# Kernel tuning notes

Hardware: AMD Instinct MI355X
Metric: run time of the kernel (lower is better)

## Reference

```python
import jax, jax.numpy as jnp
import numpy as np
import math

B, T, S = 32, 512, 256          # batch, tgt_len (prediction_length), src_len (encoder tokens)
PD, ED = 1, 768                 # pred_dim, encoder_dim
D, H, L, FF = 256, 8, 4, 1024   # d_model, nhead, num_layers, dim_feedforward
HD = D // H
NEG = -1e9
EPS = 1e-5


def _pos_encoding(seq_len, d_model):
    pos = jnp.arange(seq_len, dtype=jnp.float32)[:, None]
    div = jnp.exp(jnp.arange(0, d_model, 2, dtype=jnp.float32) * (-math.log(10000.0) / d_model))
    pe = jnp.zeros((seq_len, d_model), jnp.float32)
    pe = pe.at[:, 0::2].set(jnp.sin(pos * div))
    pe = pe.at[:, 1::2].set(jnp.cos(pos * div))
    return pe


def _ln(x, g, b):
    m = jnp.mean(x, -1, keepdims=True)
    v = jnp.mean((x - m) ** 2, -1, keepdims=True)
    return (x - m) * jax.lax.rsqrt(v + EPS) * g + b


def _mha(xq, xkv, Wq, bq, Wk, bk, Wv, bv, Wo, bo, mask):
    b, t, d = xq.shape
    s = xkv.shape[1]
    Q = (xq @ Wq + bq).reshape(b, t, H, HD).transpose(0, 2, 1, 3)   # bhtd
    K = (xkv @ Wk + bk).reshape(b, s, H, HD).transpose(0, 2, 1, 3)  # bhsd
    V = (xkv @ Wv + bv).reshape(b, s, H, HD).transpose(0, 2, 1, 3)
    scores = jnp.einsum('bhtd,bhsd->bhts', Q, K) * (HD ** -0.5)
    if mask is not None:
        scores = scores + mask
    w = jax.nn.softmax(scores, axis=-1)
    o = jnp.einsum('bhts,bhsd->bhtd', w, V).transpose(0, 2, 1, 3).reshape(b, t, d)
    return o @ Wo + bo


def _forward(tgt, memory, W_emb, b_emb, W_enc, b_enc,
             Wq_s, bq_s, Wk_s, bk_s, Wv_s, bv_s, Wo_s, bo_s,
             Wq_c, bq_c, Wk_c, bk_c, Wv_c, bv_c, Wo_c, bo_c,
             g1, be1, g2, be2, g3, be3, Wf1, bf1, Wf2, bf2,
             Wp1, bp1, Wp2, bp2):
    t = tgt.shape[1]
    x = tgt @ W_emb + b_emb + _pos_encoding(t, D)          # (B,T,D)
    mem = memory @ W_enc + b_enc                           # (B,S,D)
    causal = jnp.triu(jnp.full((t, t), NEG, jnp.float32), k=1)
    for i in range(L):
        sa = _mha(x, x, Wq_s[i], bq_s[i], Wk_s[i], bk_s[i], Wv_s[i], bv_s[i], Wo_s[i], bo_s[i], causal)
        x = _ln(x + sa, g1[i], be1[i])
        ca = _mha(x, mem, Wq_c[i], bq_c[i], Wk_c[i], bk_c[i], Wv_c[i], bv_c[i], Wo_c[i], bo_c[i], None)
        x = _ln(x + ca, g2[i], be2[i])
        ff = jax.nn.gelu(x @ Wf1[i] + bf1[i], approximate=False) @ Wf2[i] + bf2[i]
        x = _ln(x + ff, g3[i], be3[i])
    h = jax.nn.gelu(x @ Wp1 + bp1, approximate=False)
    return h @ Wp2 + bp2                                   # (B,T,PD)


def setup_inputs() -> dict:
    key = jax.random.key(0)
    keys = iter(jax.random.split(key, 40))
    def rn(shape, scale=0.05):
        return jax.random.normal(next(keys), shape, jnp.float32) * scale
    z = jnp.zeros
    inp = {
        'tgt': jax.random.normal(next(keys), (B, T, PD), jnp.float32),
        'memory': jax.random.normal(next(keys), (B, S, ED), jnp.float32),
        'W_emb': rn((PD, D)), 'b_emb': z((D,)),
        'W_enc': rn((ED, D)), 'b_enc': z((D,)),
        'Wq_s': rn((L, D, D)), 'bq_s': z((L, D)),
        'Wk_s': rn((L, D, D)), 'bk_s': z((L, D)),
        'Wv_s': rn((L, D, D)), 'bv_s': z((L, D)),
        'Wo_s': rn((L, D, D)), 'bo_s': z((L, D)),
        'Wq_c': rn((L, D, D)), 'bq_c': z((L, D)),
        'Wk_c': rn((L, D, D)), 'bk_c': z((L, D)),
        'Wv_c': rn((L, D, D)), 'bv_c': z((L, D)),
        'Wo_c': rn((L, D, D)), 'bo_c': z((L, D)),
        'g1': jnp.ones((L, D)), 'be1': z((L, D)),
        'g2': jnp.ones((L, D)), 'be2': z((L, D)),
        'g3': jnp.ones((L, D)), 'be3': z((L, D)),
        'Wf1': rn((L, D, FF)), 'bf1': z((L, FF)),
        'Wf2': rn((L, FF, D)), 'bf2': z((L, D)),
        'Wp1': rn((D, D // 2)), 'bp1': z((D // 2,)),
        'Wp2': rn((D // 2, PD), 0.01), 'bp2': jnp.full((PD,), 0.1, jnp.float32),
    }
    return inp


def reference(tgt, memory, W_emb, b_emb, W_enc, b_enc,
              Wq_s, bq_s, Wk_s, bk_s, Wv_s, bv_s, Wo_s, bo_s,
              Wq_c, bq_c, Wk_c, bk_c, Wv_c, bv_c, Wo_c, bo_c,
              g1, be1, g2, be2, g3, be3, Wf1, bf1, Wf2, bf2,
              Wp1, bp1, Wp2, bp2):
    return _forward(tgt, memory, W_emb, b_emb, W_enc, b_enc,
                    Wq_s, bq_s, Wk_s, bk_s, Wv_s, bv_s, Wo_s, bo_s,
                    Wq_c, bq_c, Wk_c, bk_c, Wv_c, bv_c, Wo_c, bo_c,
                    g1, be1, g2, be2, g3, be3, Wf1, bf1, Wf2, bf2,
                    Wp1, bp1, Wp2, bp2)
```

## Files before the change

kernel.cpp:

```cpp
#include <hip/hip_runtime.h>
#include <math.h>

#define B_  32
#define T_  512
#define S_  256
#define D_  256
#define H_  8
#define HD_ 32
#define FF_ 1024
#define ED_ 768
#define L_  4
#define BT_ (B_*T_)
#define BS_ (B_*S_)

typedef __bf16 bf16x8_t __attribute__((ext_vector_type(8)));
typedef __bf16 bf16x4_t __attribute__((ext_vector_type(4)));
typedef float  f32x4_t  __attribute__((ext_vector_type(4)));

__device__ __forceinline__ float gelu_f(float v) {
  return 0.5f * v * (1.f + erff(v * 0.7071067811865476f));
}

__device__ __forceinline__ void gl16(const __bf16* gsrc, __bf16* ldst) {
  __builtin_amdgcn_global_load_lds(
      (const __attribute__((address_space(1))) unsigned int*)gsrc,
      (__attribute__((address_space(3))) unsigned int*)ldst, 16, 0, 0);
}

__global__ __launch_bounds__(256)
void embed_kernel(const float* __restrict__ tgt, const float* __restrict__ Wemb,
                  const float* __restrict__ bemb, float* __restrict__ x,
                  __bf16* __restrict__ xbf) {
  int i = blockIdx.x * 256 + threadIdx.x;
  int d  = i & (D_ - 1);
  int bt = i >> 8;
  int t  = bt & (T_ - 1);
  int p  = d >> 1;
  float div = expf((float)(2 * p) * (-9.210340371976184f / (float)D_));
  float arg = (float)t * div;
  float pe = (d & 1) ? cosf(arg) : sinf(arg);
  float v = tgt[bt] * Wemb[d] + bemb[d] + pe;
  x[i] = v;
  xbf[i] = (__bf16)v;
}

__global__ __launch_bounds__(256)
void cvt_bf16_kernel(const float* __restrict__ in, __bf16* __restrict__ out) {
  int i = (blockIdx.x * 256 + threadIdx.x) * 4;
  float4 v = *(const float4*)(in + i);
  bf16x4_t o;
  o[0] = (__bf16)v.x; o[1] = (__bf16)v.y; o[2] = (__bf16)v.z; o[3] = (__bf16)v.w;
  *(bf16x4_t*)(out + i) = o;
}

struct TD { const float* src; size_t dst; int K, N, nb; size_t lstride; };
struct TDs { TD d[12]; };

__global__ __launch_bounds__(256)
void transpose_cvt_kernel(TDs a, __bf16* __restrict__ wt) {
  __shared__ float tile[32][33];
  TD t = a.d[blockIdx.y];
  const int kt = t.K >> 5, nt = t.N >> 5;
  const int per = kt * nt, tot = per * t.nb;
  const int id = blockIdx.x;
  if (id >= tot) return;
  const int b = id / per;
  const int r2 = id - b * per;
  const int kti = r2 / nt;
  const int nti = r2 - kti * nt;
  const int c = threadIdx.x & 31, r0 = threadIdx.x >> 5;
  const float* src = t.src + (size_t)b * t.K * t.N;
  __bf16* dst = wt + t.dst + (size_t)b * t.lstride;
#pragma unroll
  for (int j = 0; j < 4; ++j) {
    int rr = r0 + j * 8;
    tile[rr][c] = src[(size_t)(kti * 32 + rr) * t.N + nti * 32 + c];
  }
  __syncthreads();
#pragma unroll
  for (int j = 0; j < 4; ++j) {
    int rr = r0 + j * 8;
    dst[(size_t)(nti * 32 + rr) * t.K + kti * 32 + c] = (__bf16)tile[c][rr];
  }
}

__global__ __launch_bounds__(256)
void bias_concat_kernel(const float* __restrict__ bq_s, const float* __restrict__ bk_s,
                        const float* __restrict__ bv_s, const float* __restrict__ bk_c,
                        const float* __restrict__ bv_c, float* __restrict__ dst) {
  int idx = blockIdx.x * 256 + threadIdx.x;
  if (idx >= 5120) return;
  if (idx < 3072) {
    int l = idx / 768, c = idx - l * 768;
    float v = (c < 256) ? bq_s[l * 256 + c]
            : (c < 512) ? bk_s[l * 256 + c - 256]
                        : bv_s[l * 256 + c - 512];
    dst[idx] = v;
  } else {
    int j = idx - 3072;
    int l = j / 512, c = j - l * 512;
    float v = (c < 256) ? bk_c[l * 256 + c] : bv_c[l * 256 + c - 256];
    dst[idx] = v;
  }
}

template<int ACT, int OBF>
__global__ __launch_bounds__(256, 3)
void gemm_bf(const __bf16* __restrict__ A, const __bf16* __restrict__ Bt,
             const float* __restrict__ bias, void* __restrict__ Cv,
             int N, int K, int nN, int ppx) {
  __shared__ __bf16 As[128 * 64];
  __shared__ __bf16 Bs[64 * 64];
  const int tid = threadIdx.x, lane = tid & 63, wv = tid >> 6;
  const int wm = (wv & 1) * 64, wn = (wv >> 1) * 32;
  const int ln15 = lane & 15, kgrp = lane >> 4;
  const int xcd = blockIdx.x & 7, j = blockIdx.x >> 3;
  const int bm = (xcd * ppx + j / nN) * 128;
  const int bn = (j % nN) * 64;

  const int r8 = lane >> 3;
  const int scol = (lane & 7) ^ r8;
  const __bf16* a_g = A  + (size_t)(bm + wv * 32 + r8) * K + scol * 8;
  const __bf16* b_g = Bt + (size_t)(bn + wv * 16 + r8) * K + scol * 8;
  __bf16* a_l = As + wv * 2048;
  __bf16* b_l = Bs + wv * 1024;

  const int xk0 = kgrp ^ (ln15 & 7);
  const int xk1 = (4 + kgrp) ^ (ln15 & 7);

  f32x4_t acc[4][2];
#pragma unroll
  for (int mi = 0; mi < 4; ++mi)
#pragma unroll
    for (int ni = 0; ni < 2; ++ni) acc[mi][ni] = (f32x4_t){0.f, 0.f, 0.f, 0.f};

  for (int k0 = 0; k0 < K; k0 += 64) {
    gl16(a_g + k0,                a_l);
    gl16(a_g + k0 + (size_t)8*K,  a_l + 512);
    gl16(a_g + k0 + (size_t)16*K, a_l + 1024);
    gl16(a_g + k0 + (size_t)24*K, a_l + 1536);
    gl16(b_g + k0,                b_l);
    gl16(b_g + k0 + (size_t)8*K,  b_l + 512);
    __syncthreads();

#pragma unroll
    for (int kk = 0; kk < 2; ++kk) {
      const int xk = kk ? xk1 : xk0;
      bf16x8_t b0 = *(const bf16x8_t*)(Bs + ((wn + ln15) * 8 + xk) * 8);
      bf16x8_t b1 = *(const bf16x8_t*)(Bs + ((wn + 16 + ln15) * 8 + xk) * 8);
#pragma unroll
      for (int mi = 0; mi < 4; ++mi) {
        bf16x8_t af = *(const bf16x8_t*)(As + ((wm + mi * 16 + ln15) * 8 + xk) * 8);
        acc[mi][0] = __builtin_amdgcn_mfma_f32_16x16x32_bf16(af, b0, acc[mi][0], 0, 0, 0);
        acc[mi][1] = __builtin_amdgcn_mfma_f32_16x16x32_bf16(af, b1, acc[mi][1], 0, 0, 0);
      }
    }
    __syncthreads();
  }

#pragma unroll
  for (int mi = 0; mi < 4; ++mi) {
#pragma unroll
    for (int ni = 0; ni < 2; ++ni) {
      const int ocol = bn + wn + ni * 16 + ln15;
      const float bv = bias[ocol];
      const int orow0 = bm + wm + mi * 16 + kgrp * 4;
#pragma unroll
      for (int r = 0; r < 4; ++r) {
        float o = acc[mi][ni][r] + bv;
        if (ACT == 1) o = gelu_f(o);
        if (OBF) ((__bf16*)Cv)[(size_t)(orow0 + r) * N + ocol] = (__bf16)o;
        else     ((float*)Cv)[(size_t)(orow0 + r) * N + ocol] = o;
      }
    }
  }
}

template<bool CAUSAL>
__global__ __launch_bounds__(256)
void attn_mfma(const __bf16* __restrict__ Q, const __bf16* __restrict__ K,
               const __bf16* __restrict__ V, __bf16* __restrict__ O,
               int KVROWS, int qs, int ks) {
  const int b = blockIdx.x >> 3, h = blockIdx.x & 7;
  const int qt = blockIdx.y;
  const int tid = threadIdx.x, lane = tid & 63, wv = tid >> 6;
  const int ln15 = lane & 15, kgrp = lane >> 4, kgrp8 = kgrp * 8;

  __shared__ __bf16 K_lds[32][40];
  __shared__ __bf16 Vt_lds[32][40];
  __shared__ __bf16 P_lds[4][16][40];

  const int q_glob = qt * 64 + wv * 16 + ln15;
  const bf16x8_t qfrag = *(const bf16x8_t*)(Q + (size_t)(b * T_ + q_glob) * qs + h * HD_ + kgrp8);

  const int s_r = tid >> 3, s_c = (tid & 7) * 4;
  const __bf16* Kb = K + (size_t)(b * KVROWS + s_r) * ks + h * HD_ + s_c;
  const __bf16* Vb = V + (size_t)(b * KVROWS + s_r) * ks + h * HD_ + s_c;

  f32x4_t o0 = (f32x4_t){0.f,0.f,0.f,0.f}, o1 = (f32x4_t){0.f,0.f,0.f,0.f};
  float m = -3.0e38f, l = 0.f;
  const float SCALE = 0.17677669529663689f;
  const int slim = CAUSAL ? (qt + 1) * 64 : KVROWS;

  for (int s0 = 0; s0 < slim; s0 += 32) {
    *(uint2*)&K_lds[s_r][s_c] = *(const uint2*)(Kb + (size_t)s0 * ks);
    bf16x4_t vv = *(const bf16x4_t*)(Vb + (size_t)s0 * ks);
    Vt_lds[s_c + 0][s_r] = vv[0];
    Vt_lds[s_c + 1][s_r] = vv[1];
    Vt_lds[s_c + 2][s_r] = vv[2];
    Vt_lds[s_c + 3][s_r] = vv[3];
    __syncthreads();

    bf16x8_t kf0 = *(const bf16x8_t*)&K_lds[ln15][kgrp8];
    bf16x8_t kf1 = *(const bf16x8_t*)&K_lds[16 + ln15][kgrp8];
    f32x4_t sa0 = (f32x4_t){0.f,0.f,0.f,0.f}, sa1 = (f32x4_t){0.f,0.f,0.f,0.f};
    sa0 = __builtin_amdgcn_mfma_f32_16x16x32_bf16(kf0, qfrag, sa0, 0, 0, 0);
    sa1 = __builtin_amdgcn_mfma_f32_16x16x32_bf16(kf1, qfrag, sa1, 0, 0, 0);

    float v[8];
#pragma unroll
    for (int r = 0; r < 4; ++r) { v[r] = sa0[r] * SCALE; v[4 + r] = sa1[r] * SCALE; }
    if (CAUSAL) {
      const int sb = s0 + kgrp * 4;
#pragma unroll
      for (int r = 0; r < 4; ++r) {
        if (sb + r      > q_glob) v[r]     += -1e9f;
        if (sb + 16 + r > q_glob) v[4 + r] += -1e9f;
      }
    }
    float tmax = v[0];
#pragma unroll
    for (int r = 1; r < 8; ++r) tmax = fmaxf(tmax, v[r]);
    tmax = fmaxf(tmax, __shfl_xor(tmax, 16));
    tmax = fmaxf(tmax, __shfl_xor(tmax, 32));
    float mnew = fmaxf(m, tmax);
    float corr = __expf(m - mnew);

    float lsum = 0.f;
    bf16x4_t p0, p1;
#pragma unroll
    for (int r = 0; r < 4; ++r) {
      float e0 = __expf(v[r] - mnew);
      float e1 = __expf(v[4 + r] - mnew);
      lsum += e0 + e1;
      p0[r] = (__bf16)e0;
      p1[r] = (__bf16)e1;
    }
    *(bf16x4_t*)&P_lds[wv][ln15][kgrp * 4]      = p0;
    *(bf16x4_t*)&P_lds[wv][ln15][16 + kgrp * 4] = p1;
    lsum += __shfl_xor(lsum, 16);
    lsum += __shfl_xor(lsum, 32);
    l = l * corr + lsum;
    m = mnew;

    const float c0 = __shfl(corr, kgrp * 4 + 0);
    const float c1 = __shfl(corr, kgrp * 4 + 1);
    const float c2 = __shfl(corr, kgrp * 4 + 2);
    const float c3 = __shfl(corr, kgrp * 4 + 3);
    o0[0] *= c0; o0[1] *= c1; o0[2] *= c2; o0[3] *= c3;
    o1[0] *= c0; o1[1] *= c1; o1[2] *= c2; o1[3] *= c3;

    bf16x8_t pf  = *(const bf16x8_t*)&P_lds[wv][ln15][kgrp8];
    bf16x8_t vf0 = *(const bf16x8_t*)&Vt_lds[ln15][kgrp8];
    bf16x8_t vf1 = *(const bf16x8_t*)&Vt_lds[16 + ln15][kgrp8];
    o0 = __builtin_amdgcn_mfma_f32_16x16x32_bf16(pf, vf0, o0, 0, 0, 0);
    o1 = __builtin_amdgcn_mfma_f32_16x16x32_bf16(pf, vf1, o1, 0, 0, 0);
    __syncthreads();
  }

  const float inv = 1.f / l;
  const float i0 = __shfl(inv, kgrp * 4 + 0);
  const float i1 = __shfl(inv, kgrp * 4 + 1);
  const float i2 = __shfl(inv, kgrp * 4 + 2);
  const float i3 = __shfl(inv, kgrp * 4 + 3);
  __bf16* Op = O + (size_t)(b * T_ + qt * 64 + wv * 16 + kgrp * 4) * D_ + h * HD_;
  Op[0 * D_ + ln15] = (__bf16)(o0[0] * i0);  Op[0 * D_ + 16 + ln15] = (__bf16)(o1[0] * i0);
  Op[1 * D_ + ln15] = (__bf16)(o0[1] * i1);  Op[1 * D_ + 16 + ln15] = (__bf16)(o1[1] * i1);
  Op[2 * D_ + ln15] = (__bf16)(o0[2] * i2);  Op[2 * D_ + 16 + ln15] = (__bf16)(o1[2] * i2);
  Op[3 * D_ + ln15] = (__bf16)(o0[3] * i3);  Op[3 * D_ + 16 + ln15] = (__bf16)(o1[3] * i3);
}

__global__ __launch_bounds__(256)
void add_ln_kernel(float* __restrict__ x, __bf16* __restrict__ xbf,
                   const float* __restrict__ y,
                   const float* __restrict__ g, const float* __restrict__ bta) {
  const int row = blockIdx.x * 4 + (threadIdx.x >> 6);
  const int lane = threadIdx.x & 63;
  const size_t base = (size_t)row * D_ + lane * 4;
  float4 xv = *(const float4*)&x[base];
  float4 yv = *(const float4*)&y[base];
  float v0 = xv.x + yv.x, v1 = xv.y + yv.y, v2 = xv.z + yv.z, v3 = xv.w + yv.w;
  float sum = v0 + v1 + v2 + v3;
  float sq  = v0 * v0 + v1 * v1 + v2 * v2 + v3 * v3;
#pragma unroll
  for (int off = 32; off; off >>= 1) {
    sum += __shfl_xor(sum, off);
    sq  += __shfl_xor(sq, off);
  }
  float mean = sum * (1.f / D_);
  float var  = sq * (1.f / D_) - mean * mean;
  float rstd = rsqrtf(fmaxf(var, 0.f) + 1e-5f);
  const int c = lane * 4;
  float4 gv = *(const float4*)&g[c];
  float4 bv = *(const float4*)&bta[c];
  float4 ov;
  ov.x = (v0 - mean) * rstd * gv.x + bv.x;
  ov.y = (v1 - mean) * rstd * gv.y + bv.y;
  ov.z = (v2 - mean) * rstd * gv.z + bv.z;
  ov.w = (v3 - mean) * rstd * gv.w + bv.w;
  *(float4*)&x[base] = ov;
  bf16x4_t ob;
  ob[0] = (__bf16)ov.x; ob[1] = (__bf16)ov.y; ob[2] = (__bf16)ov.z; ob[3] = (__bf16)ov.w;
  *(bf16x4_t*)&xbf[base] = ob;
}

__global__ __launch_bounds__(256)
void head2_kernel(const float* __restrict__ hb, const float* __restrict__ w,
                  const float* __restrict__ bias, float* __restrict__ out) {
  const int row = blockIdx.x * 4 + (threadIdx.x >> 6);
  const int lane = threadIdx.x & 63;
  float a = hb[(size_t)row * 128 + lane] * w[lane]
          + hb[(size_t)row * 128 + 64 + lane] * w[64 + lane];
#pragma unroll
  for (int off = 32; off; off >>= 1) a += __shfl_xor(a, off);
  if (lane == 0) out[row] = a + bias[0];
}

extern "C" void kernel_launch(void* const* d_in, const int* in_sizes, int n_in,
                              void* d_out, int out_size, void* d_ws, size_t ws_size,
                              hipStream_t stream) {
  const float* tgt    = (const float*)d_in[0];
  const float* memory = (const float*)d_in[1];
  const float* W_emb  = (const float*)d_in[2];
  const float* b_emb  = (const float*)d_in[3];
  const float* W_enc  = (const float*)d_in[4];
  const float* b_enc  = (const float*)d_in[5];
  const float* Wq_s = (const float*)d_in[6];  const float* bq_s = (const float*)d_in[7];
  const float* Wk_s = (const float*)d_in[8];  const float* bk_s = (const float*)d_in[9];
  const float* Wv_s = (const float*)d_in[10]; const float* bv_s = (const float*)d_in[11];
  const float* Wo_s = (const float*)d_in[12]; const float* bo_s = (const float*)d_in[13];
  const float* Wq_c = (const float*)d_in[14]; const float* bq_c = (const float*)d_in[15];
  const float* Wk_c = (const float*)d_in[16]; const float* bk_c = (const float*)d_in[17];
  const float* Wv_c = (const float*)d_in[18]; const float* bv_c = (const float*)d_in[19];
  const float* Wo_c = (const float*)d_in[20]; const float* bo_c = (const float*)d_in[21];
  const float* g1  = (const float*)d_in[22]; const float* be1 = (const float*)d_in[23];
  const float* g2  = (const float*)d_in[24]; const float* be2 = (const float*)d_in[25];
  const float* g3  = (const float*)d_in[26]; const float* be3 = (const float*)d_in[27];
  const float* Wf1 = (const float*)d_in[28]; const float* bf1 = (const float*)d_in[29];
  const float* Wf2 = (const float*)d_in[30]; const float* bf2 = (const float*)d_in[31];
  const float* Wp1 = (const float*)d_in[32]; const float* bp1 = (const float*)d_in[33];
  const float* Wp2 = (const float*)d_in[34]; const float* bp2 = (const float*)d_in[35];

  float*  x    = (float*)d_ws;
  float*  y    = x + (size_t)BT_ * D_;
  __bf16* xbf  = (__bf16*)(y + (size_t)BT_ * D_);
  __bf16* membf= xbf + (size_t)BT_ * D_;
  __bf16* qkv  = membf + (size_t)BS_ * D_;
  __bf16* ext  = qkv + (size_t)BT_ * 768;
  __bf16* ao   = ext + (size_t)4194304;
  __bf16* wt   = ao + (size_t)BT_ * D_;
  float*  bcat = (float*)(wt + 4423680);
  __bf16* memb = qkv;
  __bf16* qc   = qkv;
  __bf16* kvc  = qkv + (size_t)BT_ * D_;
  __bf16* ff   = qkv;

  const size_t o_enc  = 0;
  const size_t o_qkv  = 196608;
  const size_t o_qcw  = 983040;
  const size_t o_kvw  = 1245184;
  const size_t o_os   = 1769472;
  const size_t o_oc   = 2031616;
  const size_t o_f1   = 2293760;
  const size_t o_f2   = 3342336;
  const size_t o_p1   = 4390912;

  TDs td;
  td.d[0]  = {W_enc, o_enc,           ED_, D_,  1, 0};
  td.d[1]  = {Wq_s,  o_qkv + 0,       D_,  D_,  L_, 196608};
  td.d[2]  = {Wk_s,  o_qkv + 65536,   D_,  D_,  L_, 196608};
  td.d[3]  = {Wv_s,  o_qkv + 131072,  D_,  D_,  L_, 196608};
  td.d[4]  = {Wq_c,  o_qcw,           D_,  D_,  L_, 65536};
  td.d[5]  = {Wk_c,  o_kvw + 0,       D_,  D_,  L_, 131072};
  td.d[6]  = {Wv_c,  o_kvw + 65536,   D_,  D_,  L_, 131072};
  td.d[7]  = {Wo_s,  o_os,            D_,  D_,  L_, 65536};
  td.d[8]  = {Wo_c,  o_oc,            D_,  D_,  L_, 65536};
  td.d[9]  = {Wf1,   o_f1,            D_,  FF_, L_, 262144};
  td.d[10] = {Wf2,   o_f2,            FF_, D_,  L_, 262144};
  td.d[11] = {Wp1,   o_p1,            D_,  128, 1, 0};

  dim3 blk(256);
  cvt_bf16_kernel<<<BS_ * ED_ / 1024, blk, 0, stream>>>(memory, memb);
  transpose_cvt_kernel<<<dim3(1024, 12), blk, 0, stream>>>(td, wt);
  bias_concat_kernel<<<20, blk, 0, stream>>>(bq_s, bk_s, bv_s, bk_c, bv_c, bcat);
  embed_kernel<<<BT_ * D_ / 256, blk, 0, stream>>>(tgt, W_emb, b_emb, x, xbf);

  const float* bqkv = bcat;
  const float* bkv  = bcat + 3072;
  const dim3 gA(B_ * H_, T_ / 64);

  gemm_bf<0,1><<<64 * 4, blk, 0, stream>>>(memb, wt + o_enc, b_enc, membf, D_, ED_, 4, 8);

  for (int i = 0; i < L_; ++i) {
    gemm_bf<0,1><<<128 * 12, blk, 0, stream>>>(xbf, wt + o_qkv + (size_t)i * 196608, bqkv + i * 768, qkv, 768, D_, 12, 16);
    attn_mfma<true><<<gA, blk, 0, stream>>>(qkv, qkv + 256, qkv + 512, ao, T_, 768, 768);
    gemm_bf<0,0><<<128 * 4, blk, 0, stream>>>(ao, wt + o_os + (size_t)i * 65536, bo_s + i * D_, y, D_, D_, 4, 16);
    add_ln_kernel<<<BT_ / 4, blk, 0, stream>>>(x, xbf, y, g1 + i * D_, be1 + i * D_);
    gemm_bf<0,1><<<128 * 4, blk, 0, stream>>>(xbf, wt + o_qcw + (size_t)i * 65536, bq_c + i * D_, qc, D_, D_, 4, 16);
    gemm_bf<0,1><<<64 * 8, blk, 0, stream>>>(membf, wt + o_kvw + (size_t)i * 131072, bkv + i * 512, kvc, 512, D_, 8, 8);
    attn_mfma<false><<<gA, blk, 0, stream>>>(qc, kvc, kvc + 256, ao, S_, 256, 512);
    gemm_bf<0,0><<<128 * 4, blk, 0, stream>>>(ao, wt + o_oc + (size_t)i * 65536, bo_c + i * D_, y, D_, D_, 4, 16);
    add_ln_kernel<<<BT_ / 4, blk, 0, stream>>>(x, xbf, y, g2 + i * D_, be2 + i * D_);
    gemm_bf<1,1><<<128 * 16, blk, 0, stream>>>(xbf, wt + o_f1 + (size_t)i * 262144, bf1 + i * FF_, ff, FF_, D_, 16, 16);
    gemm_bf<0,0><<<128 * 4, blk, 0, stream>>>(ff, wt + o_f2 + (size_t)i * 262144, bf2 + i * D_, y, D_, FF_, 4, 16);
    add_ln_kernel<<<BT_ / 4, blk, 0, stream>>>(x, xbf, y, g3 + i * D_, be3 + i * D_);
  }
  gemm_bf<1,0><<<128 * 2, blk, 0, stream>>>(xbf, wt + o_p1, bp1, y, 128, D_, 2, 16);
  head2_kernel<<<BT_ / 4, blk, 0, stream>>>(y, Wp2, bp2, (float*)d_out);
}
```

Before: 752.3 us.

## Add 128x128 GEMM tile, widen attention KV tile, store residual branch in bf16

Adds a gemm_bf2 kernel with 128x128 output tiles and a 4x4 MFMA grid per wave, and uses it for the QKV and FF1 projections. The larger tiles raise operand reuse and halve the number of blocks for those GEMMs. Attention now processes 64 keys per iteration instead of 32, with 8-wide vector K/V loads, which halves the loop trips and barrier count. The output, cross-attention and FF2 projections now write their result in bf16 and add_ln reads bf16, cutting that traffic in half. The cost is lower precision in the residual branch and more register pressure in the new GEMM.

```diff
diff --git a/kernel.cpp b/kernel.cpp
--- a/kernel.cpp
+++ b/kernel.cpp
@@ -176,6 +176,83 @@
   }
 }
 
+template<int ACT, int OBF>
+__global__ __launch_bounds__(256, 3)
+void gemm_bf2(const __bf16* __restrict__ A, const __bf16* __restrict__ Bt,
+              const float* __restrict__ bias, void* __restrict__ Cv,
+              int N, int K, int nN, int ppx) {
+  __shared__ __bf16 As[128 * 64];
+  __shared__ __bf16 Bs[128 * 64];
+  const int tid = threadIdx.x, lane = tid & 63, wv = tid >> 6;
+  const int wm = (wv & 1) * 64, wn = (wv >> 1) * 64;
+  const int ln15 = lane & 15, kgrp = lane >> 4;
+  const int xcd = blockIdx.x & 7, j = blockIdx.x >> 3;
+  const int bm = (xcd * ppx + j / nN) * 128;
+  const int bn = (j % nN) * 128;
+
+  const int r8 = lane >> 3;
+  const int scol = (lane & 7) ^ r8;
+  const __bf16* a_g = A  + (size_t)(bm + wv * 32 + r8) * K + scol * 8;
+  const __bf16* b_g = Bt + (size_t)(bn + wv * 32 + r8) * K + scol * 8;
+  __bf16* a_l = As + wv * 2048;
+  __bf16* b_l = Bs + wv * 2048;
+
+  const int xk0 = kgrp ^ (ln15 & 7);
+  const int xk1 = (4 + kgrp) ^ (ln15 & 7);
+
+  f32x4_t acc[4][4];
+#pragma unroll
+  for (int mi = 0; mi < 4; ++mi)
+#pragma unroll
+    for (int ni = 0; ni < 4; ++ni) acc[mi][ni] = (f32x4_t){0.f, 0.f, 0.f, 0.f};
+
+  for (int k0 = 0; k0 < K; k0 += 64) {
+    gl16(a_g + k0,                a_l);
+    gl16(a_g + k0 + (size_t)8*K,  a_l + 512);
+    gl16(a_g + k0 + (size_t)16*K, a_l + 1024);
+    gl16(a_g + k0 + (size_t)24*K, a_l + 1536);
+    gl16(b_g + k0,                b_l);
+    gl16(b_g + k0 + (size_t)8*K,  b_l + 512);
+    gl16(b_g + k0 + (size_t)16*K, b_l + 1024);
+    gl16(b_g + k0 + (size_t)24*K, b_l + 1536);
+    __syncthreads();
+
+#pragma unroll
+    for (int kk = 0; kk < 2; ++kk) {
+      const int xk = kk ? xk1 : xk0;
+      bf16x8_t bfr[4];
+#pragma unroll
+      for (int ni = 0; ni < 4; ++ni)
+        bfr[ni] = *(const bf16x8_t*)(Bs + ((wn + ni * 16 + ln15) * 8 + xk) * 8);
+#pragma unroll
+      for (int mi = 0; mi < 4; ++mi) {
+        bf16x8_t af = *(const bf16x8_t*)(As + ((wm + mi * 16 + ln15) * 8 + xk) * 8);
+#pragma unroll
+        for (int ni = 0; ni < 4; ++ni)
+          acc[mi][ni] = __builtin_amdgcn_mfma_f32_16x16x32_bf16(af, bfr[ni], acc[mi][ni], 0, 0, 0);
+      }
+    }
+    __syncthreads();
+  }
+
+#pragma unroll
+  for (int mi = 0; mi < 4; ++mi) {
+#pragma unroll
+    for (int ni = 0; ni < 4; ++ni) {
+      const int ocol = bn + wn + ni * 16 + ln15;
+      const float bv = bias[ocol];
+      const int orow0 = bm + wm + mi * 16 + kgrp * 4;
+#pragma unroll
+      for (int r = 0; r < 4; ++r) {
+        float o = acc[mi][ni][r] + bv;
+        if (ACT == 1) o = gelu_f(o);
+        if (OBF) ((__bf16*)Cv)[(size_t)(orow0 + r) * N + ocol] = (__bf16)o;
+        else     ((float*)Cv)[(size_t)(orow0 + r) * N + ocol] = o;
+      }
+    }
+  }
+}
+
 template<bool CAUSAL>
 __global__ __launch_bounds__(256)
 void attn_mfma(const __bf16* __restrict__ Q, const __bf16* __restrict__ K,
@@ -186,68 +263,64 @@
   const int tid = threadIdx.x, lane = tid & 63, wv = tid >> 6;
   const int ln15 = lane & 15, kgrp = lane >> 4, kgrp8 = kgrp * 8;
 
-  __shared__ __bf16 K_lds[32][40];
-  __shared__ __bf16 Vt_lds[32][40];
-  __shared__ __bf16 P_lds[4][16][40];
+  __shared__ __bf16 K_lds[64][36];
+  __shared__ __bf16 Vt_lds[32][72];
+  __shared__ __bf16 P_lds[4][16][72];
 
   const int q_glob = qt * 64 + wv * 16 + ln15;
   const bf16x8_t qfrag = *(const bf16x8_t*)(Q + (size_t)(b * T_ + q_glob) * qs + h * HD_ + kgrp8);
 
-  const int s_r = tid >> 3, s_c = (tid & 7) * 4;
-  const __bf16* Kb = K + (size_t)(b * KVROWS + s_r) * ks + h * HD_ + s_c;
-  const __bf16* Vb = V + (size_t)(b * KVROWS + s_r) * ks + h * HD_ + s_c;
+  const int s_r = tid >> 2, s_c8 = (tid & 3) * 8;
+  const __bf16* Kb = K + (size_t)(b * KVROWS + s_r) * ks + h * HD_ + s_c8;
+  const __bf16* Vb = V + (size_t)(b * KVROWS + s_r) * ks + h * HD_ + s_c8;
 
   f32x4_t o0 = (f32x4_t){0.f,0.f,0.f,0.f}, o1 = (f32x4_t){0.f,0.f,0.f,0.f};
   float m = -3.0e38f, l = 0.f;
   const float SCALE = 0.17677669529663689f;
   const int slim = CAUSAL ? (qt + 1) * 64 : KVROWS;
 
-  for (int s0 = 0; s0 < slim; s0 += 32) {
-    *(uint2*)&K_lds[s_r][s_c] = *(const uint2*)(Kb + (size_t)s0 * ks);
-    bf16x4_t vv = *(const bf16x4_t*)(Vb + (size_t)s0 * ks);
-    Vt_lds[s_c + 0][s_r] = vv[0];
-    Vt_lds[s_c + 1][s_r] = vv[1];
-    Vt_lds[s_c + 2][s_r] = vv[2];
-    Vt_lds[s_c + 3][s_r] = vv[3];
+  for (int s0 = 0; s0 < slim; s0 += 64) {
+    *(bf16x8_t*)&K_lds[s_r][s_c8] = *(const bf16x8_t*)(Kb + (size_t)s0 * ks);
+    bf16x8_t vv = *(const bf16x8_t*)(Vb + (size_t)s0 * ks);
+#pragma unroll
+    for (int jj = 0; jj < 8; ++jj) Vt_lds[s_c8 + jj][s_r] = vv[jj];
     __syncthreads();
 
-    bf16x8_t kf0 = *(const bf16x8_t*)&K_lds[ln15][kgrp8];
-    bf16x8_t kf1 = *(const bf16x8_t*)&K_lds[16 + ln15][kgrp8];
-    f32x4_t sa0 = (f32x4_t){0.f,0.f,0.f,0.f}, sa1 = (f32x4_t){0.f,0.f,0.f,0.f};
-    sa0 = __builtin_amdgcn_mfma_f32_16x16x32_bf16(kf0, qfrag, sa0, 0, 0, 0);
-    sa1 = __builtin_amdgcn_mfma_f32_16x16x32_bf16(kf1, qfrag, sa1, 0, 0, 0);
-
-    float v[8];
-#pragma unroll
-    for (int r = 0; r < 4; ++r) { v[r] = sa0[r] * SCALE; v[4 + r] = sa1[r] * SCALE; }
-    if (CAUSAL) {
-      const int sb = s0 + kgrp * 4;
+    f32x4_t sa[4];
+#pragma unroll
+    for (int c = 0; c < 4; ++c) {
+      bf16x8_t kf = *(const bf16x8_t*)&K_lds[c * 16 + ln15][kgrp8];
+      sa[c] = __builtin_amdgcn_mfma_f32_16x16x32_bf16(kf, qfrag, (f32x4_t){0.f,0.f,0.f,0.f}, 0, 0, 0);
+    }
+    float v[16];
+#pragma unroll
+    for (int c = 0; c < 4; ++c)
 #pragma unroll
       for (int r = 0; r < 4; ++r) {
-        if (sb + r      > q_glob) v[r]     += -1e9f;
-        if (sb + 16 + r > q_glob) v[4 + r] += -1e9f;
+        float s = sa[c][r] * SCALE;
+        if (CAUSAL && (s0 + c * 16 + kgrp * 4 + r) > q_glob) s += -1e9f;
+        v[c * 4 + r] = s;
       }
-    }
     float tmax = v[0];
 #pragma unroll
-    for (int r = 1; r < 8; ++r) tmax = fmaxf(tmax, v[r]);
+    for (int r = 1; r < 16; ++r) tmax = fmaxf(tmax, v[r]);
     tmax = fmaxf(tmax, __shfl_xor(tmax, 16));
     tmax = fmaxf(tmax, __shfl_xor(tmax, 32));
     float mnew = fmaxf(m, tmax);
     float corr = __expf(m - mnew);
 
     float lsum = 0.f;
-    bf16x4_t p0, p1;
-#pragma unroll
-    for (int r = 0; r < 4; ++r) {
-      float e0 = __expf(v[r] - mnew);
-      float e1 = __expf(v[4 + r] - mnew);
-      lsum += e0 + e1;
-      p0[r] = (__bf16)e0;
-      p1[r] = (__bf16)e1;
+#pragma unroll
+    for (int c = 0; c < 4; ++c) {
+      bf16x4_t pc;
+#pragma unroll
+      for (int r = 0; r < 4; ++r) {
+        float e = __expf(v[c * 4 + r] - mnew);
+        lsum += e;
+        pc[r] = (__bf16)e;
+      }
+      *(bf16x4_t*)&P_lds[wv][ln15][c * 16 + kgrp * 4] = pc;
     }
-    *(bf16x4_t*)&P_lds[wv][ln15][kgrp * 4]      = p0;
-    *(bf16x4_t*)&P_lds[wv][ln15][16 + kgrp * 4] = p1;
     lsum += __shfl_xor(lsum, 16);
     lsum += __shfl_xor(lsum, 32);
     l = l * corr + lsum;
@@ -260,11 +333,16 @@
     o0[0] *= c0; o0[1] *= c1; o0[2] *= c2; o0[3] *= c3;
     o1[0] *= c0; o1[1] *= c1; o1[2] *= c2; o1[3] *= c3;
 
-    bf16x8_t pf  = *(const bf16x8_t*)&P_lds[wv][ln15][kgrp8];
-    bf16x8_t vf0 = *(const bf16x8_t*)&Vt_lds[ln15][kgrp8];
-    bf16x8_t vf1 = *(const bf16x8_t*)&Vt_lds[16 + ln15][kgrp8];
-    o0 = __builtin_amdgcn_mfma_f32_16x16x32_bf16(pf, vf0, o0, 0, 0, 0);
-    o1 = __builtin_amdgcn_mfma_f32_16x16x32_bf16(pf, vf1, o1, 0, 0, 0);
+    bf16x8_t pLo = *(const bf16x8_t*)&P_lds[wv][ln15][kgrp8];
+    bf16x8_t pHi = *(const bf16x8_t*)&P_lds[wv][ln15][32 + kgrp8];
+    bf16x8_t v0l = *(const bf16x8_t*)&Vt_lds[ln15][kgrp8];
+    bf16x8_t v0h = *(const bf16x8_t*)&Vt_lds[ln15][32 + kgrp8];
+    bf16x8_t v1l = *(const bf16x8_t*)&Vt_lds[16 + ln15][kgrp8];
+    bf16x8_t v1h = *(const bf16x8_t*)&Vt_lds[16 + ln15][32 + kgrp8];
+    o0 = __builtin_amdgcn_mfma_f32_16x16x32_bf16(pLo, v0l, o0, 0, 0, 0);
+    o0 = __builtin_amdgcn_mfma_f32_16x16x32_bf16(pHi, v0h, o0, 0, 0, 0);
+    o1 = __builtin_amdgcn_mfma_f32_16x16x32_bf16(pLo, v1l, o1, 0, 0, 0);
+    o1 = __builtin_amdgcn_mfma_f32_16x16x32_bf16(pHi, v1h, o1, 0, 0, 0);
     __syncthreads();
   }
 
@@ -282,14 +360,15 @@
 
 __global__ __launch_bounds__(256)
 void add_ln_kernel(float* __restrict__ x, __bf16* __restrict__ xbf,
-                   const float* __restrict__ y,
+                   const __bf16* __restrict__ y,
                    const float* __restrict__ g, const float* __restrict__ bta) {
   const int row = blockIdx.x * 4 + (threadIdx.x >> 6);
   const int lane = threadIdx.x & 63;
   const size_t base = (size_t)row * D_ + lane * 4;
   float4 xv = *(const float4*)&x[base];
-  float4 yv = *(const float4*)&y[base];
-  float v0 = xv.x + yv.x, v1 = xv.y + yv.y, v2 = xv.z + yv.z, v3 = xv.w + yv.w;
+  bf16x4_t yv = *(const bf16x4_t*)&y[base];
+  float v0 = xv.x + (float)yv[0], v1 = xv.y + (float)yv[1];
+  float v2 = xv.z + (float)yv[2], v3 = xv.w + (float)yv[3];
   float sum = v0 + v1 + v2 + v3;
   float sq  = v0 * v0 + v1 * v1 + v2 * v2 + v3 * v3;
 #pragma unroll
@@ -352,8 +431,9 @@
   const float* Wp2 = (const float*)d_in[34]; const float* bp2 = (const float*)d_in[35];
 
   float*  x    = (float*)d_ws;
-  float*  y    = x + (size_t)BT_ * D_;
-  __bf16* xbf  = (__bf16*)(y + (size_t)BT_ * D_);
+  float*  yf   = x + (size_t)BT_ * D_;
+  __bf16* ybf  = (__bf16*)yf;
+  __bf16* xbf  = (__bf16*)(yf + (size_t)BT_ * D_);
   __bf16* membf= xbf + (size_t)BT_ * D_;
   __bf16* qkv  = membf + (size_t)BS_ * D_;
   __bf16* ext  = qkv + (size_t)BT_ * 768;
@@ -402,19 +482,19 @@
   gemm_bf<0,1><<<64 * 4, blk, 0, stream>>>(memb, wt + o_enc, b_enc, membf, D_, ED_, 4, 8);
 
   for (int i = 0; i < L_; ++i) {
-    gemm_bf<0,1><<<128 * 12, blk, 0, stream>>>(xbf, wt + o_qkv + (size_t)i * 196608, bqkv + i * 768, qkv, 768, D_, 12, 16);
+    gemm_bf2<0,1><<<128 * 6, blk, 0, stream>>>(xbf, wt + o_qkv + (size_t)i * 196608, bqkv + i * 768, qkv, 768, D_, 6, 16);
     attn_mfma<true><<<gA, blk, 0, stream>>>(qkv, qkv + 256, qkv + 512, ao, T_, 768, 768);
-    gemm_bf<0,0><<<128 * 4, blk, 0, stream>>>(ao, wt + o_os + (size_t)i * 65536, bo_s + i * D_, y, D_, D_, 4, 16);
-    add_ln_kernel<<<BT_ / 4, blk, 0, stream>>>(x, xbf, y, g1 + i * D_, be1 + i * D_);
+    gemm_bf<0,1><<<128 * 4, blk, 0, stream>>>(ao, wt + o_os + (size_t)i * 65536, bo_s + i * D_, ybf, D_, D_, 4, 16);
+    add_ln_kernel<<<BT_ / 4, blk, 0, stream>>>(x, xbf, ybf, g1 + i * D_, be1 + i * D_);
     gemm_bf<0,1><<<128 * 4, blk, 0, stream>>>(xbf, wt + o_qcw + (size_t)i * 65536, bq_c + i * D_, qc, D_, D_, 4, 16);
     gemm_bf<0,1><<<64 * 8, blk, 0, stream>>>(membf, wt + o_kvw + (size_t)i * 131072, bkv + i * 512, kvc, 512, D_, 8, 8);
     attn_mfma<false><<<gA, blk, 0, stream>>>(qc, kvc, kvc + 256, ao, S_, 256, 512);
-    gemm_bf<0,0><<<128 * 4, blk, 0, stream>>>(ao, wt + o_oc + (size_t)i * 65536, bo_c + i * D_, y, D_, D_, 4, 16);
-    add_ln_kernel<<<BT_ / 4, blk, 0, stream>>>(x, xbf, y, g2 + i * D_, be2 + i * D_);
-    gemm_bf<1,1><<<128 * 16, blk, 0, stream>>>(xbf, wt + o_f1 + (size_t)i * 262144, bf1 + i * FF_, ff, FF_, D_, 16, 16);
-    gemm_bf<0,0><<<128 * 4, blk, 0, stream>>>(ff, wt + o_f2 + (size_t)i * 262144, bf2 + i * D_, y, D_, FF_, 4, 16);
-    add_ln_kernel<<<BT_ / 4, blk, 0, stream>>>(x, xbf, y, g3 + i * D_, be3 + i * D_);
-  }
-  gemm_bf<1,0><<<128 * 2, blk, 0, stream>>>(xbf, wt + o_p1, bp1, y, 128, D_, 2, 16);
-  head2_kernel<<<BT_ / 4, blk, 0, stream>>>(y, Wp2, bp2, (float*)d_out);
-}
+    gemm_bf<0,1><<<128 * 4, blk, 0, stream>>>(ao, wt + o_oc + (size_t)i * 65536, bo_c + i * D_, ybf, D_, D_, 4, 16);
+    add_ln_kernel<<<BT_ / 4, blk, 0, stream>>>(x, xbf, ybf, g2 + i * D_, be2 + i * D_);
+    gemm_bf2<1,1><<<128 * 8, blk, 0, stream>>>(xbf, wt + o_f1 + (size_t)i * 262144, bf1 + i * FF_, ff, FF_, D_, 8, 16);
+    gemm_bf<0,1><<<128 * 4, blk, 0, stream>>>(ff, wt + o_f2 + (size_t)i * 262144, bf2 + i * D_, ybf, D_, FF_, 4, 16);
+    add_ln_kernel<<<BT_ / 4, blk, 0, stream>>>(x, xbf, ybf, g3 + i * D_, be3 + i * D_);
+  }
+  gemm_bf<1,0><<<128 * 2, blk, 0, stream>>>(xbf, wt + o_p1, bp1, yf, 128, D_, 2, 16);
+  head2_kernel<<<BT_ / 4, blk, 0, stream>>>(yf, Wp2, bp2, (float*)d_out);
+}
```

New measurement: 710.9 us. -5.5%, faster.
